# Performance work log

Hardware: AMD Instinct MI355X
Metric: run time of the kernel (lower is better)

## Reference

```python
import jax, jax.numpy as jnp
import numpy as np

EMBED = 32; HEADS = 4; HD = 8; FFN = 64; OBS = 64; CTX = 128; BATCH = 16
INIT_SCALE = 1.0 / np.sqrt(2.0 * 5.0)  # 1/sqrt(2*(3 spatial + 2 temporal))


def rmsnorm(x, w, eps=1e-6):
    return x / jnp.sqrt(jnp.mean(x * x, axis=-1, keepdims=True) + eps) * w


def rope_cache(T):
    theta = 1.0 / (10000.0 ** (jnp.arange(0, HD, 2, dtype=jnp.float32) / HD))
    freqs = jnp.arange(T, dtype=jnp.float32)[:, None] * theta[None, :]  # [T, HD//2]
    return jnp.cos(freqs), jnp.sin(freqs)


def apply_rope(x, cos, sin):
    half = x.shape[-1] // 2
    x1, x2 = x[..., :half], x[..., half:]
    c, s = cos[None, None], sin[None, None]  # broadcast over [B, H, T, HD//2]
    return jnp.concatenate([x1 * c - x2 * s, x2 * c + x1 * s], axis=-1)


def attn_block(x, Wq, Wk, Wv, Wo, Wg, Wval, Wout, norm4, qkn, cos=None, sin=None):
    B, S, W = x.shape
    h = rmsnorm(x, norm4[0])

    def proj(Wm):
        return jnp.einsum('bsw,dw->bsd', h, Wm).reshape(B, S, HEADS, HD).transpose(0, 2, 1, 3)

    q = rmsnorm(proj(Wq), qkn[0])
    k = rmsnorm(proj(Wk), qkn[1])
    v = proj(Wv)
    if cos is not None:
        q = apply_rope(q, cos, sin)
        k = apply_rope(k, cos, sin)
    scores = jnp.einsum('bhqd,bhkd->bhqk', q, k) / np.float32(np.sqrt(HD))
    o = jnp.einsum('bhqk,bhkd->bhqd', jax.nn.softmax(scores, axis=-1), v)
    o = o.transpose(0, 2, 1, 3).reshape(B, S, W)
    x = x + rmsnorm(jnp.einsum('bsw,dw->bsd', o, Wo), norm4[1])
    h2 = rmsnorm(x, norm4[2])
    ffn = jax.nn.silu(jnp.einsum('bsw,fw->bsf', h2, Wg)) * jnp.einsum('bsw,fw->bsf', h2, Wval)
    x = x + rmsnorm(jnp.einsum('bsf,wf->bsw', ffn, Wout), norm4[3])
    return x


def setup_inputs():
    key = jax.random.key(0)
    ks = iter(jax.random.split(key, 40))
    sd = 1.0 / np.sqrt(EMBED)
    inp = {
        'obs_seq': jax.random.normal(next(ks), (BATCH, CTX, OBS), jnp.float32),
        'W_val': jax.random.normal(next(ks), (EMBED, 1), jnp.float32),
        'b_val': jnp.zeros((EMBED,), jnp.float32),
        'input_norm_w': jnp.ones((EMBED,), jnp.float32),
        'dim_embed': jax.random.normal(next(ks), (OBS, EMBED), jnp.float32),
        'cls_tokens': jax.random.normal(next(ks), (3, EMBED), jnp.float32) * sd,
        'final_norm_w': jnp.ones((EMBED,), jnp.float32),
    }
    for pre, n in (('s', 3), ('t', 2)):
        inp[pre + '_Wq'] = jax.random.normal(next(ks), (n, EMBED, EMBED), jnp.float32) * sd
        inp[pre + '_Wk'] = jax.random.normal(next(ks), (n, EMBED, EMBED), jnp.float32) * sd
        inp[pre + '_Wv'] = jax.random.normal(next(ks), (n, EMBED, EMBED), jnp.float32) * sd
        inp[pre + '_Wo'] = jax.random.normal(next(ks), (n, EMBED, EMBED), jnp.float32) * (0.1 * INIT_SCALE * sd)
        inp[pre + '_Wg'] = jax.random.normal(next(ks), (n, FFN, EMBED), jnp.float32) * sd
        inp[pre + '_Wval'] = jax.random.normal(next(ks), (n, FFN, EMBED), jnp.float32) * sd
        inp[pre + '_Wout'] = jax.random.normal(next(ks), (n, EMBED, FFN), jnp.float32) * (INIT_SCALE / np.sqrt(FFN))
        inp[pre + '_norm4'] = jnp.ones((n, 4, EMBED), jnp.float32)
        inp[pre + '_qkn'] = jnp.ones((n, 2, HD), jnp.float32)
    return inp


def reference(obs_seq, W_val, b_val, input_norm_w, dim_embed, cls_tokens, final_norm_w,
              s_Wq, s_Wk, s_Wv, s_Wo, s_Wg, s_Wval, s_Wout, s_norm4, s_qkn,
              t_Wq, t_Wk, t_Wv, t_Wo, t_Wg, t_Wval, t_Wout, t_norm4, t_qkn):
    B, T, D = obs_seq.shape
    slots = D + 3
    # value_proj: Linear(1, EMBED) applied to each scalar feature
    tok = obs_seq[..., None] * W_val[:, 0] + b_val            # [B, T, D, EMBED]
    tok = tok + dim_embed[None, None]                          # dim id embedding
    cls = jnp.broadcast_to(cls_tokens[None, None], (B, T, 3, EMBED))
    tokens = rmsnorm(jnp.concatenate([tok, cls], axis=2), input_norm_w)  # [B,T,slots,EMBED]
    cos, sin = rope_cache(T)

    def spatial(tk, i):
        x = tk.reshape(B * T, slots, EMBED)
        x = attn_block(x, s_Wq[i], s_Wk[i], s_Wv[i], s_Wo[i], s_Wg[i], s_Wval[i], s_Wout[i], s_norm4[i], s_qkn[i])
        return x.reshape(B, T, slots, EMBED)

    def temporal(tk, i):
        x = tk.transpose(0, 2, 1, 3).reshape(B * slots, T, EMBED)
        x = attn_block(x, t_Wq[i], t_Wk[i], t_Wv[i], t_Wo[i], t_Wg[i], t_Wval[i], t_Wout[i], t_norm4[i], t_qkn[i], cos, sin)
        return x.reshape(B, slots, T, EMBED).transpose(0, 2, 1, 3)

    tokens = spatial(tokens, 0)
    tokens = temporal(tokens, 0)
    tokens = spatial(tokens, 1)
    tokens = temporal(tokens, 1)
    tokens = spatial(tokens, 2)
    tokens = rmsnorm(tokens, final_norm_w)
    last = tokens[:, -1]  # [B, slots, EMBED]
    return last[:, D], last[:, D + 1], last[:, D + 2]
```

## Files before the change

### kernel.cpp

```cpp
#include <hip/hip_runtime.h>

#define B_ 16
#define T_ 128
#define OBS_ 64
#define SLOTS_ 67
#define E_ 32
#define H_ 4
#define HD_ 8
#define FFN_ 64

typedef _Float16 h2 __attribute__((ext_vector_type(2)));
typedef _Float16 h4 __attribute__((ext_vector_type(4)));
typedef _Float16 h8 __attribute__((ext_vector_type(8)));
typedef __fp16 mh4 __attribute__((ext_vector_type(4)));
typedef __fp16 mh8 __attribute__((ext_vector_type(8)));
typedef float fx4 __attribute__((ext_vector_type(4)));
union H4u { h4 v; h2 h[2]; };

#define WBLK 10240
#define X16_BYTES (B_ * T_ * SLOTS_ * E_ * 2)
#define W16_BYTES (5 * WBLK * 2)
#define ROPE_OFF (X16_BYTES + W16_BYTES)
#define EMBED_BLOCKS ((B_ * T_ * SLOTS_ + 7) / 8)

__device__ __forceinline__ float red32(float v) {
  v += __shfl_xor(v, 16); v += __shfl_xor(v, 8); v += __shfl_xor(v, 4);
  v += __shfl_xor(v, 2);  v += __shfl_xor(v, 1);
  return v;
}
template <int CTRL>
__device__ __forceinline__ float dpp_add(float v) {
  int s = __builtin_amdgcn_update_dpp(0, __builtin_bit_cast(int, v), CTRL,
                                      0xF, 0xF, true);
  return v + __builtin_bit_cast(float, s);
}
__device__ __forceinline__ float red8(float v) {
  v = dpp_add<0xB1>(v);
  v = dpp_add<0x4E>(v);
  v = dpp_add<0x141>(v);
  return v;
}
__device__ __forceinline__ float bfly16(float v) {
  v = dpp_add<0xB1>(v);
  v = dpp_add<0x4E>(v);
  v = dpp_add<0x141>(v);
  v = dpp_add<0x140>(v);
  return v;
}
__device__ __forceinline__ h2 pkrtz(float x, float y) {
  return __builtin_bit_cast(h2, __builtin_amdgcn_cvt_pkrtz(x, y));
}
__device__ __forceinline__ float rcp_(float x) { return __builtin_amdgcn_rcpf(x); }
__device__ __forceinline__ float rsq_(float x) { return __builtin_amdgcn_rsqf(x); }
__device__ __forceinline__ fx4 mfma16(h8 a, h8 b, fx4 c) {
  return __builtin_amdgcn_mfma_f32_16x16x32_f16(
      __builtin_bit_cast(mh8, a), __builtin_bit_cast(mh8, b), c, 0, 0, 0);
}
__device__ __forceinline__ fx4 mfma16k16(h4 a, h4 b, fx4 c) {
  return __builtin_amdgcn_mfma_f32_16x16x16f16(
      __builtin_bit_cast(mh4, a), __builtin_bit_cast(mh4, b), c, 0, 0, 0);
}

__device__ __forceinline__ int sw32(int row, int col) {
  return row * 32 + (col ^ (((row >> 1) & 3) << 3));
}
__device__ __forceinline__ int sw64(int row, int col) {
  return row * 64 + (col ^ ((row & 7) << 3));
}

struct WPtrs {
  const float *sWq, *sWk, *sWv, *sWo, *sWg, *sWvl, *sWout;
  const float *tWq, *tWk, *tWv, *tWo, *tWg, *tWvl, *tWout;
};

#define CVT_BLOCKS 100

__global__ __launch_bounds__(256) void setup_kernel(
    WPtrs p, _Float16* __restrict__ dst,
    const float* __restrict__ obs, const float* __restrict__ Wval,
    const float* __restrict__ bval, const float* __restrict__ innw,
    const float* __restrict__ dimemb, const float* __restrict__ cls,
    float2* __restrict__ rope, _Float16* __restrict__ X) {
  if (blockIdx.x < CVT_BLOCKS) {
    int i = blockIdx.x * 256 + threadIdx.x;
    const int total_pairs = 5 * WBLK / 2;
    if (i >= total_pairs) return;
    int blk = i / (WBLK / 2);
    int f = (i % (WBLK / 2)) * 2;
    bool sp = blk < 3;
    int bi = sp ? blk : blk - 3;
    const float* src;
    int o;
    if (f < 1024)      { src = (sp ? p.sWq : p.tWq) + bi * 1024;  o = f; }
    else if (f < 2048) { src = (sp ? p.sWk : p.tWk) + bi * 1024;  o = f - 1024; }
    else if (f < 3072) { src = (sp ? p.sWv : p.tWv) + bi * 1024;  o = f - 2048; }
    else if (f < 4096) { src = (sp ? p.sWo : p.tWo) + bi * 1024;  o = f - 3072; }
    else if (f < 6144) { src = (sp ? p.sWg : p.tWg) + bi * 2048;  o = f - 4096; }
    else if (f < 8192) { src = (sp ? p.sWvl : p.tWvl) + bi * 2048; o = f - 6144; }
    else               { src = (sp ? p.sWout : p.tWout) + bi * 2048; o = f - 8192; }
    ((h2*)dst)[i] = pkrtz(src[o], src[o + 1]);
  } else if (blockIdx.x < CVT_BLOCKS + EMBED_BLOCKS) {
    int tok = (blockIdx.x - CVT_BLOCKS) * 8 + (threadIdx.x >> 5);
    int e = threadIdx.x & 31;
    const int total = B_ * T_ * SLOTS_;
    if (tok >= total) return;
    int slot = tok % SLOTS_;
    int bt = tok / SLOTS_;
    float v;
    if (slot < OBS_) {
      float o = obs[bt * OBS_ + slot];
      v = o * Wval[e] + bval[e] + dimemb[slot * E_ + e];
    } else {
      v = cls[(slot - OBS_) * E_ + e];
    }
    float ss = red32(v * v);
    X[tok * E_ + e] = (_Float16)(v * rsq_(ss * (1.0f / E_) + 1e-6f) * innw[e]);
  } else {
    for (int i = threadIdx.x; i < T_ * 4; i += 256) {
      int pos = i >> 2, j = i & 3;
      float th = __builtin_amdgcn_exp2f(-(float)j * 3.3219280948873623f);
      float sv, cv;
      __sincosf((float)pos * th, &sv, &cv);
      rope[i] = make_float2(cv, sv);
    }
  }
}

template <int SV, int SP, bool TEMPORAL, bool LAST>
__device__ __forceinline__ void block_body(
    _Float16* __restrict__ X, const _Float16* __restrict__ W16,
    const float* __restrict__ norm4, const float* __restrict__ qkn,
    const float2* __restrict__ rope, const float* __restrict__ fnw,
    float* __restrict__ out, int bid) {
  constexpr int MT = SP / 16;
  constexpr int MTW = (MT + 3) / 4;
  constexpr int VSTRIDE = TEMPORAL ? 128 : 168;
  constexpr int VROWS = TEMPORAL ? 32 : 33;
  __shared__ __align__(16) _Float16 smem[SP * 96 + VROWS * VSTRIDE];
  _Float16* hb = smem;
  _Float16* qb = smem + SP * 32;
  _Float16* kb = smem + SP * 64;
  _Float16* vT = smem + SP * 96;
  _Float16* ffnb = qb;

  const int tid = threadIdx.x;
  const int l = tid & 63, wv = tid >> 6;
  const int lm = l & 15, lq = l >> 4, hd = l & 7;

  auto vt_idx = [](int d, int s) {
    if (TEMPORAL) return d * 128 + (((s & ~15) ^ ((d & 7) << 4)) | (s & 15));
    return d * VSTRIDE + s;
  };

  int base, stride;
  if (TEMPORAL) {
    int b = bid / SLOTS_;
    int slot = bid % SLOTS_;
    base = (b * T_ * SLOTS_ + slot) * E_;
    stride = SLOTS_ * E_;
  } else {
    base = bid * 2 * SLOTS_ * E_;
    stride = E_;
  }

  const float nw0a = norm4[lm],      nw0b = norm4[16 + lm];
  const float nw1a = norm4[32 + lm], nw1b = norm4[48 + lm];
  const float nw2a = norm4[64 + lm], nw2b = norm4[80 + lm];
  const float nw3a = norm4[96 + lm], nw3b = norm4[112 + lm];
  const fx4 fz = {0.f, 0.f, 0.f, 0.f};
  const float qw = qkn[hd], kw = qkn[8 + hd];
  const float qscale = 0.35355339059327373f * 1.4426950408889634f;

  float xr[MTW][4][2];
#pragma unroll
  for (int t = 0; t < MTW; t++) {
    int mt = wv + 4 * t;
    if (mt < MT) {
#pragma unroll
      for (int r = 0; r < 4; r++) {
        int s = mt * 16 + lq * 4 + r;
        bool ok = (SV == SP) || (s < SV);
        int off = base + s * stride;
        xr[t][r][0] = ok ? (float)X[off + lm] : 0.f;
        xr[t][r][1] = ok ? (float)X[off + 16 + lm] : 0.f;
      }
    }
  }
#pragma unroll
  for (int t = 0; t < MTW; t++) {
    int mt = wv + 4 * t;
    if (mt < MT) {
#pragma unroll
      for (int r = 0; r < 4; r++) {
        int s = mt * 16 + lq * 4 + r;
        float p = bfly16(xr[t][r][0] * xr[t][r][0] + xr[t][r][1] * xr[t][r][1]);
        float inv = rsq_(p * (1.0f / E_) + 1e-6f);
        if (SV == SP || s < SV) {
          hb[sw32(s, lm)] = (_Float16)(xr[t][r][0] * inv * nw0a);
          hb[sw32(s, 16 + lm)] = (_Float16)(xr[t][r][1] * inv * nw0b);
        }
      }
    }
  }
  __syncthreads();

  for (int u = wv; u < MT * 2; u += 4) {
    const int mt = u >> 1, nt = u & 1;
    h8 aH = *(const h8*)(hb + sw32(mt * 16 + lm, lq * 8));
    float rc[4], rs[4];
    if (TEMPORAL) {
#pragma unroll
      for (int r = 0; r < 4; r++) {
        float2 cs = rope[(mt * 16 + lq * 4 + r) * 4 + (hd & 3)];
        rc[r] = cs.x; rs[r] = cs.y;
      }
    }
    const int d = nt * 16 + lm;
    h8 bq = *(const h8*)(W16 + (nt * 16 + lm) * 32 + lq * 8);
    h8 bk = *(const h8*)(W16 + 1024 + (nt * 16 + lm) * 32 + lq * 8);
    h8 bv = *(const h8*)(W16 + 2048 + (nt * 16 + lm) * 32 + lq * 8);
    fx4 aq = mfma16(aH, bq, fz);
    fx4 ak = mfma16(aH, bk, fz);
    fx4 av = mfma16(aH, bv, fz);
#pragma unroll
    for (int r = 0; r < 4; r++) {
      int s = mt * 16 + lq * 4 + r;
      float q1 = aq[r], k1 = ak[r];
      float qv = q1 * rsq_(red8(q1 * q1) * 0.125f + 1e-6f) * qw;
      float kv = k1 * rsq_(red8(k1 * k1) * 0.125f + 1e-6f) * kw;
      if (TEMPORAL) {
        float qp = __shfl_xor(qv, 4);
        float kp = __shfl_xor(kv, 4);
        qv = (hd < 4) ? (qv * rc[r] - qp * rs[r]) : (qv * rc[r] + qp * rs[r]);
        kv = (hd < 4) ? (kv * rc[r] - kp * rs[r]) : (kv * rc[r] + kp * rs[r]);
      }
      if (SV == SP || s < SV) {
        qb[sw32(s, d)] = (_Float16)(qv * qscale);
        kb[sw32(s, d)] = (_Float16)kv;
      }
    }
    const int s0 = mt * 16 + lq * 4;
    const int va = vt_idx(d, s0);
    if (SV == SP || s0 + 1 < SV) *(h2*)(vT + va) = pkrtz(av[0], av[1]);
    if (SV == SP || s0 + 3 < SV) *(h2*)(vT + va + 2) = pkrtz(av[2], av[3]);
  }
  if (!TEMPORAL) {
    for (int idx = tid; idx < 32 * 13; idx += 256) {
      int d = idx / 13, c = 2 * SLOTS_ + 2 * (idx % 13);
      *(h2*)(vT + d * VSTRIDE + c) = pkrtz(0.f, 0.f);
    }
    for (int idx = tid; idx < VSTRIDE / 2; idx += 256) {
      *(h2*)(vT + 32 * VSTRIDE + 2 * idx) = pkrtz(1.f, 1.f);
    }
  }
  __syncthreads();

  {
    const int h = wv;
    const h8 z8 = {};
    const h4 ones4 = {(_Float16)1.f, (_Float16)1.f, (_Float16)1.f, (_Float16)1.f};
    const bool vlane = (lm < 8);
    const int dv = h * 8 + (lm & 7);
    const int vrow = (!TEMPORAL && !vlane) ? 32 : dv;

    auto loadK = [&](int kt) {
      return *(const h8*)(kb + sw32(kt * 16 + lm, lq * 8));
    };
    auto loadV = [&](int kt) {
      h4 v = *(const h4*)(vT + vt_idx(vrow, kt * 16 + lq * 4));
      return (TEMPORAL && !vlane) ? ones4 : v;
    };
    auto loadQ = [&](int mt) {
      h8 b = *(const h8*)(qb + sw32(mt * 16 + lm, lq * 8));
      return (lq == h) ? b : z8;
    };
    auto maskx = [&](float x, int kidx, int mode, int q) {
      if (mode == 1) return (kidx < SLOTS_) ? x : 0.f;
      if (mode == 2) return (kidx >= SLOTS_) ? x : 0.f;
      if (mode == 3) return (kidx < 2 * SLOTS_) ? x : 0.f;
      if (mode == 4) {
        bool ok = (kidx < 2 * SLOTS_) && ((kidx < SLOTS_) == (q < SLOTS_));
        return ok ? x : 0.f;
      }
      return x;
    };
    auto pvstep = [&](const h4& av, int kt, int mode, int q, const fx4& sc,
                      fx4& oacc) {
      float ev[4];
#pragma unroll
      for (int r = 0; r < 4; r++) {
        int kidx = kt * 16 + lq * 4 + r;
        ev[r] = maskx(__builtin_amdgcn_exp2f(sc[r]), kidx, mode, q);
      }
      H4u pT;
      pT.h[0] = pkrtz(ev[0], ev[1]); pT.h[1] = pkrtz(ev[2], ev[3]);
      oacc = mfma16k16(av, pT.v, oacc);
    };
    auto finish = [&](int mt, fx4& oa) {
      int q = mt * 16 + lm;
      float lsum = __shfl_xor(oa[0], 32);
      float inv = rcp_(lsum);
      if (lq < 2 && (SV == SP || q < SV)) {
        H4u ov;
        ov.h[0] = pkrtz(oa[0] * inv, oa[1] * inv);
        ov.h[1] = pkrtz(oa[2] * inv, oa[3] * inv);
        *(h4*)(hb + sw32(q, h * 8 + lq * 4)) = ov.v;
      }
    };

    if (TEMPORAL) {
      h8 aK[MT]; h4 aV[MT];
#pragma unroll
      for (int kt = 0; kt < MT; kt++) { aK[kt] = loadK(kt); aV[kt] = loadV(kt); }
#pragma unroll
      for (int mtp = 0; mtp < MT / 2; mtp++) {
        h8 bQ0 = loadQ(2 * mtp), bQ1 = loadQ(2 * mtp + 1);
        fx4 o0 = fz, o1 = fz;
#pragma unroll
        for (int kt = 0; kt < MT; kt++) {
          fx4 s0 = mfma16(aK[kt], bQ0, fz);
          fx4 s1 = mfma16(aK[kt], bQ1, fz);
          pvstep(aV[kt], kt, 0, 0, s0, o0);
          pvstep(aV[kt], kt, 0, 0, s1, o1);
        }
        finish(2 * mtp, o0);
        finish(2 * mtp + 1, o1);
      }
    } else {
      {
        h8 aKw[5]; h4 aVw[5];
#pragma unroll
        for (int kt = 0; kt < 5; kt++) { aKw[kt] = loadK(kt); aVw[kt] = loadV(kt); }
#pragma unroll
        for (int mtp = 0; mtp < 2; mtp++) {
          h8 bQ0 = loadQ(2 * mtp), bQ1 = loadQ(2 * mtp + 1);
          fx4 o0 = fz, o1 = fz;
#pragma unroll
          for (int kt = 0; kt < 5; kt++) {
            int mode = (kt == 4) ? 1 : 0;
            fx4 s0 = mfma16(aKw[kt], bQ0, fz);
            fx4 s1 = mfma16(aKw[kt], bQ1, fz);
            pvstep(aVw[kt], kt, mode, 0, s0, o0);
            pvstep(aVw[kt], kt, mode, 0, s1, o1);
          }
          finish(2 * mtp, o0);
          finish(2 * mtp + 1, o1);
        }
      }
      {
        h8 aKw[9]; h4 aVw[9];
#pragma unroll
        for (int kt = 0; kt < 9; kt++) { aKw[kt] = loadK(kt); aVw[kt] = loadV(kt); }
        h8 bQ = loadQ(4);
        fx4 oa = fz;
        const int q = 4 * 16 + lm;
#pragma unroll
        for (int kt = 0; kt < 9; kt++) {
          fx4 sc = mfma16(aKw[kt], bQ, fz);
          pvstep(aVw[kt], kt, 4, q, sc, oa);
        }
        finish(4, oa);
      }
      {
        h8 aKw[5]; h4 aVw[5];
#pragma unroll
        for (int kt = 0; kt < 5; kt++) {
          aKw[kt] = loadK(kt + 4); aVw[kt] = loadV(kt + 4);
        }
#pragma unroll
        for (int mtp = 0; mtp < 2; mtp++) {
          int m0 = 5 + 2 * mtp;
          h8 bQ0 = loadQ(m0), bQ1 = loadQ(m0 + 1);
          fx4 o0 = fz, o1 = fz;
#pragma unroll
          for (int kt = 0; kt < 5; kt++) {
            int mode = (kt == 0) ? 2 : (kt == 4 ? 3 : 0);
            fx4 s0 = mfma16(aKw[kt], bQ0, fz);
            fx4 s1 = mfma16(aKw[kt], bQ1, fz);
            pvstep(aVw[kt], kt + 4, mode, 0, s0, o0);
            pvstep(aVw[kt], kt + 4, mode, 0, s1, o1);
          }
          finish(m0, o0);
          finish(m0 + 1, o1);
        }
      }
    }
  }
  __syncthreads();

#pragma unroll
  for (int t = 0; t < MTW; t++) {
    int mt = wv + 4 * t;
    if (mt < MT) {
      h8 aO = *(const h8*)(hb + sw32(mt * 16 + lm, lq * 8));
      h8 b0 = *(const h8*)(W16 + 3072 + lm * 32 + lq * 8);
      h8 b1 = *(const h8*)(W16 + 3072 + (16 + lm) * 32 + lq * 8);
      fx4 a0 = mfma16(aO, b0, fz);
      fx4 a1 = mfma16(aO, b1, fz);
#pragma unroll
      for (int r = 0; r < 4; r++) {
        int s = mt * 16 + lq * 4 + r;
        float p = bfly16(a0[r] * a0[r] + a1[r] * a1[r]);
        float inv = rsq_(p * (1.0f / E_) + 1e-6f);
        xr[t][r][0] += a0[r] * inv * nw1a;
        xr[t][r][1] += a1[r] * inv * nw1b;
        float q2 = bfly16(xr[t][r][0] * xr[t][r][0] + xr[t][r][1] * xr[t][r][1]);
        float inv2 = rsq_(q2 * (1.0f / E_) + 1e-6f);
        if (SV == SP || s < SV) {
          hb[sw32(s, lm)] = (_Float16)(xr[t][r][0] * inv2 * nw2a);
          hb[sw32(s, 16 + lm)] = (_Float16)(xr[t][r][1] * inv2 * nw2b);
        }
      }
    }
  }
  __syncthreads();

  for (int u = wv; u < MT * 4; u += 4) {
    const int mt = u >> 2, nt = u & 3;
    h8 aH2 = *(const h8*)(hb + sw32(mt * 16 + lm, lq * 8));
    h8 bg = *(const h8*)(W16 + 4096 + (nt * 16 + lm) * 32 + lq * 8);
    h8 bl = *(const h8*)(W16 + 6144 + (nt * 16 + lm) * 32 + lq * 8);
    fx4 g = mfma16(aH2, bg, fz);
    fx4 vvv = mfma16(aH2, bl, fz);
#pragma unroll
    for (int r = 0; r < 4; r++) {
      int s = mt * 16 + lq * 4 + r;
      if (SV == SP || s < SV) {
        float gg = g[r];
        float sg = gg * rcp_(1.0f + __builtin_amdgcn_exp2f(gg * -1.4426950408889634f));
        ffnb[sw64(s, nt * 16 + lm)] = (_Float16)(sg * vvv[r]);
      }
    }
  }
  __syncthreads();

#pragma unroll
  for (int t = 0; t < MTW; t++) {
    int mt = wv + 4 * t;
    if (mt < MT) {
      const int row = mt * 16 + lm;
      h8 a0 = *(const h8*)(ffnb + sw64(row, lq * 8));
      h8 a1 = *(const h8*)(ffnb + sw64(row, 32 + lq * 8));
      h8 b00 = *(const h8*)(W16 + 8192 + lm * 64 + lq * 8);
      h8 b01 = *(const h8*)(W16 + 8192 + lm * 64 + 32 + lq * 8);
      h8 b10 = *(const h8*)(W16 + 8192 + (16 + lm) * 64 + lq * 8);
      h8 b11 = *(const h8*)(W16 + 8192 + (16 + lm) * 64 + 32 + lq * 8);
      fx4 o0 = mfma16(a1, b01, mfma16(a0, b00, fz));
      fx4 o1 = mfma16(a1, b11, mfma16(a0, b10, fz));
#pragma unroll
      for (int r = 0; r < 4; r++) {
        int s = mt * 16 + lq * 4 + r;
        float p = bfly16(o0[r] * o0[r] + o1[r] * o1[r]);
        float inv = rsq_(p * (1.0f / E_) + 1e-6f);
        xr[t][r][0] += o0[r] * inv * nw3a;
        xr[t][r][1] += o1[r] * inv * nw3b;
        if (SV == SP || s < SV) {
          int off = base + s * stride;
          X[off + lm] = (_Float16)xr[t][r][0];
          X[off + 16 + lm] = (_Float16)xr[t][r][1];
        }
      }
      if (LAST && mt == MT - 1 && (bid & (T_ / 2 - 1)) == (T_ / 2 - 1)) {
        const int b = bid / (T_ / 2);
#pragma unroll
        for (int r = 0; r < 4; r++) {
          int s = mt * 16 + lq * 4 + r;
          int j = s - (SLOTS_ + OBS_);
          float p2 = bfly16(xr[t][r][0] * xr[t][r][0] + xr[t][r][1] * xr[t][r][1]);
          if (j >= 0 && j < 3) {
            float inv2 = rsq_(p2 * (1.0f / E_) + 1e-6f);
            out[j * (B_ * E_) + b * E_ + lm] = xr[t][r][0] * inv2 * fnw[lm];
            out[j * (B_ * E_) + b * E_ + 16 + lm] = xr[t][r][1] * inv2 * fnw[16 + lm];
          }
        }
      }
    }
  }
}

__global__ __launch_bounds__(256, 4) void attn_spatial_kernel(
    _Float16* __restrict__ X, const _Float16* __restrict__ W16,
    const float* __restrict__ norm4, const float* __restrict__ qkn) {
  block_body<2 * SLOTS_, 144, false, false>(X, W16, norm4, qkn, nullptr,
                                            nullptr, nullptr, blockIdx.x);
}

__global__ __launch_bounds__(256, 4) void attn_spatial_last_kernel(
    _Float16* __restrict__ X, const _Float16* __restrict__ W16,
    const float* __restrict__ norm4, const float* __restrict__ qkn,
    const float* __restrict__ fnw, float* __restrict__ out) {
  block_body<2 * SLOTS_, 144, false, true>(X, W16, norm4, qkn, nullptr,
                                           fnw, out, blockIdx.x);
}

__global__ __launch_bounds__(256, 4) void attn_temporal_kernel(
    _Float16* __restrict__ X, const _Float16* __restrict__ W16,
    const float* __restrict__ norm4, const float* __restrict__ qkn,
    const float2* __restrict__ rope) {
  block_body<T_, 128, true, false>(X, W16, norm4, qkn, rope,
                                   nullptr, nullptr, blockIdx.x);
}

extern "C" void kernel_launch(void* const* d_in, const int* in_sizes, int n_in,
                              void* d_out, int out_size, void* d_ws, size_t ws_size,
                              hipStream_t stream) {
  (void)in_sizes; (void)n_in; (void)out_size; (void)ws_size;
  const float* obs          = (const float*)d_in[0];
  const float* W_val        = (const float*)d_in[1];
  const float* b_val        = (const float*)d_in[2];
  const float* input_norm_w = (const float*)d_in[3];
  const float* dim_embed    = (const float*)d_in[4];
  const float* cls_tokens   = (const float*)d_in[5];
  const float* final_norm_w = (const float*)d_in[6];
  const float* s_n4   = (const float*)d_in[14];
  const float* s_qkn  = (const float*)d_in[15];
  const float* t_n4   = (const float*)d_in[23];
  const float* t_qkn  = (const float*)d_in[24];

  _Float16* X = (_Float16*)d_ws;
  _Float16* W16 = (_Float16*)((char*)d_ws + X16_BYTES);
  float2* rope = (float2*)((char*)d_ws + ROPE_OFF);
  float* out = (float*)d_out;

  WPtrs wp;
  wp.sWq   = (const float*)d_in[7];
  wp.sWk   = (const float*)d_in[8];
  wp.sWv   = (const float*)d_in[9];
  wp.sWo   = (const float*)d_in[10];
  wp.sWg   = (const float*)d_in[11];
  wp.sWvl  = (const float*)d_in[12];
  wp.sWout = (const float*)d_in[13];
  wp.tWq   = (const float*)d_in[16];
  wp.tWk   = (const float*)d_in[17];
  wp.tWv   = (const float*)d_in[18];
  wp.tWo   = (const float*)d_in[19];
  wp.tWg   = (const float*)d_in[20];
  wp.tWvl  = (const float*)d_in[21];
  wp.tWout = (const float*)d_in[22];

  setup_kernel<<<CVT_BLOCKS + EMBED_BLOCKS + 1, 256, 0, stream>>>(
      wp, W16, obs, W_val, b_val, input_norm_w, dim_embed, cls_tokens, rope, X);

  const int N4 = 4 * E_;
  const int QN = 2 * HD_;

#define SPATIAL(i)                                                     \
  attn_spatial_kernel<<<B_ * T_ / 2, 256, 0, stream>>>(                \
      X, W16 + (i)*WBLK, s_n4 + (i)*N4, s_qkn + (i)*QN)
#define TEMPORAL(i)                                                    \
  attn_temporal_kernel<<<B_ * SLOTS_, 256, 0, stream>>>(               \
      X, W16 + (3 + (i)) * WBLK, t_n4 + (i)*N4, t_qkn + (i)*QN, rope)

  SPATIAL(0);
  TEMPORAL(0);
  SPATIAL(1);
  TEMPORAL(1);
  attn_spatial_last_kernel<<<B_ * T_ / 2, 256, 0, stream>>>(
      X, W16 + 2 * WBLK, s_n4 + 2 * N4, s_qkn + 2 * QN, final_norm_w, out);

#undef SPATIAL
#undef TEMPORAL
}
```

Before: 281.8 us.

## Process one spatial group per block instead of packing two

The spatial kernel now gives each block a single 67-token group, padded to 80 rows, instead of packing two groups into 144 rows. Grid size doubles and per-block shared memory shrinks. The block-diagonal masking modes go away, and the middle tile's wasted cross-group work is no longer computed. The cost is lower MFMA tile utilisation (67 of 80 rows) and twice as many blocks to schedule.

Result: slower. 289.1 us (+2.6%).

```diff
diff --git a/kernel.cpp b/kernel.cpp
--- a/kernel.cpp
+++ b/kernel.cpp
@@ -134,7 +134,7 @@
     float* __restrict__ out, int bid) {
   constexpr int MT = SP / 16;
   constexpr int MTW = (MT + 3) / 4;
-  constexpr int VSTRIDE = TEMPORAL ? 128 : 168;
+  constexpr int VSTRIDE = TEMPORAL ? 128 : 88;
   constexpr int VROWS = TEMPORAL ? 32 : 33;
   __shared__ __align__(16) _Float16 smem[SP * 96 + VROWS * VSTRIDE];
   _Float16* hb = smem;
@@ -159,7 +159,7 @@
     base = (b * T_ * SLOTS_ + slot) * E_;
     stride = SLOTS_ * E_;
   } else {
-    base = bid * 2 * SLOTS_ * E_;
+    base = bid * SLOTS_ * E_;
     stride = E_;
   }
 
@@ -243,14 +243,15 @@
     const int va = vt_idx(d, s0);
     if (SV == SP || s0 + 1 < SV) *(h2*)(vT + va) = pkrtz(av[0], av[1]);
     if (SV == SP || s0 + 3 < SV) *(h2*)(vT + va + 2) = pkrtz(av[2], av[3]);
+    else if (s0 + 2 < SV)        *(h2*)(vT + va + 2) = pkrtz(av[2], 0.f);
   }
   if (!TEMPORAL) {
-    for (int idx = tid; idx < 32 * 13; idx += 256) {
-      int d = idx / 13, c = 2 * SLOTS_ + 2 * (idx % 13);
-      *(h2*)(vT + d * VSTRIDE + c) = pkrtz(0.f, 0.f);
-    }
-    for (int idx = tid; idx < VSTRIDE / 2; idx += 256) {
-      *(h2*)(vT + 32 * VSTRIDE + 2 * idx) = pkrtz(1.f, 1.f);
+    for (int idx = tid; idx < 32 * (SP - SV); idx += 256) {
+      int d = idx / (SP - SV), c = SV + idx % (SP - SV);
+      vT[d * VSTRIDE + c] = (_Float16)0.f;
+    }
+    for (int idx = tid; idx < SP; idx += 256) {
+      vT[32 * VSTRIDE + idx] = (_Float16)1.f;
     }
   }
   __syncthreads();
@@ -274,23 +275,17 @@
       h8 b = *(const h8*)(qb + sw32(mt * 16 + lm, lq * 8));
       return (lq == h) ? b : z8;
     };
-    auto maskx = [&](float x, int kidx, int mode, int q) {
+    auto maskx = [&](float x, int kidx, int mode) {
       if (mode == 1) return (kidx < SLOTS_) ? x : 0.f;
-      if (mode == 2) return (kidx >= SLOTS_) ? x : 0.f;
-      if (mode == 3) return (kidx < 2 * SLOTS_) ? x : 0.f;
-      if (mode == 4) {
-        bool ok = (kidx < 2 * SLOTS_) && ((kidx < SLOTS_) == (q < SLOTS_));
-        return ok ? x : 0.f;
-      }
       return x;
     };
-    auto pvstep = [&](const h4& av, int kt, int mode, int q, const fx4& sc,
+    auto pvstep = [&](const h4& av, int kt, int mode, const fx4& sc,
                       fx4& oacc) {
       float ev[4];
 #pragma unroll
       for (int r = 0; r < 4; r++) {
         int kidx = kt * 16 + lq * 4 + r;
-        ev[r] = maskx(__builtin_amdgcn_exp2f(sc[r]), kidx, mode, q);
+        ev[r] = maskx(__builtin_amdgcn_exp2f(sc[r]), kidx, mode);
       }
       H4u pT;
       pT.h[0] = pkrtz(ev[0], ev[1]); pT.h[1] = pkrtz(ev[2], ev[3]);
@@ -320,69 +315,42 @@
         for (int kt = 0; kt < MT; kt++) {
           fx4 s0 = mfma16(aK[kt], bQ0, fz);
           fx4 s1 = mfma16(aK[kt], bQ1, fz);
-          pvstep(aV[kt], kt, 0, 0, s0, o0);
-          pvstep(aV[kt], kt, 0, 0, s1, o1);
+          pvstep(aV[kt], kt, 0, s0, o0);
+          pvstep(aV[kt], kt, 0, s1, o1);
         }
         finish(2 * mtp, o0);
         finish(2 * mtp + 1, o1);
       }
     } else {
+      h8 aKw[5]; h4 aVw[5];
+#pragma unroll
+      for (int kt = 0; kt < 5; kt++) { aKw[kt] = loadK(kt); aVw[kt] = loadV(kt); }
+#pragma unroll
+      for (int mtp = 0; mtp < 2; mtp++) {
+        h8 bQ0 = loadQ(2 * mtp), bQ1 = loadQ(2 * mtp + 1);
+        fx4 o0 = fz, o1 = fz;
+#pragma unroll
+        for (int kt = 0; kt < 5; kt++) {
+          int mode = (kt == 4) ? 1 : 0;
+          fx4 s0 = mfma16(aKw[kt], bQ0, fz);
+          fx4 s1 = mfma16(aKw[kt], bQ1, fz);
+          pvstep(aVw[kt], kt, mode, s0, o0);
+          pvstep(aVw[kt], kt, mode, s1, o1);
+        }
+        finish(2 * mtp, o0);
+        finish(2 * mtp + 1, o1);
+      }
       {
-        h8 aKw[5]; h4 aVw[5];
-#pragma unroll
-        for (int kt = 0; kt < 5; kt++) { aKw[kt] = loadK(kt); aVw[kt] = loadV(kt); }
-#pragma unroll
-        for (int mtp = 0; mtp < 2; mtp++) {
-          h8 bQ0 = loadQ(2 * mtp), bQ1 = loadQ(2 * mtp + 1);
-          fx4 o0 = fz, o1 = fz;
-#pragma unroll
-          for (int kt = 0; kt < 5; kt++) {
-            int mode = (kt == 4) ? 1 : 0;
-            fx4 s0 = mfma16(aKw[kt], bQ0, fz);
-            fx4 s1 = mfma16(aKw[kt], bQ1, fz);
-            pvstep(aVw[kt], kt, mode, 0, s0, o0);
-            pvstep(aVw[kt], kt, mode, 0, s1, o1);
-          }
-          finish(2 * mtp, o0);
-          finish(2 * mtp + 1, o1);
-        }
-      }
-      {
-        h8 aKw[9]; h4 aVw[9];
-#pragma unroll
-        for (int kt = 0; kt < 9; kt++) { aKw[kt] = loadK(kt); aVw[kt] = loadV(kt); }
         h8 bQ = loadQ(4);
-        fx4 oa = fz;
-        const int q = 4 * 16 + lm;
-#pragma unroll
-        for (int kt = 0; kt < 9; kt++) {
+        fx4 oa = fz, ob = fz;
+#pragma unroll
+        for (int kt = 0; kt < 5; kt++) {
+          int mode = (kt == 4) ? 1 : 0;
           fx4 sc = mfma16(aKw[kt], bQ, fz);
-          pvstep(aVw[kt], kt, 4, q, sc, oa);
-        }
+          pvstep(aVw[kt], kt, mode, sc, (kt & 1) ? ob : oa);
+        }
+        oa = oa + ob;
         finish(4, oa);
-      }
-      {
-        h8 aKw[5]; h4 aVw[5];
-#pragma unroll
-        for (int kt = 0; kt < 5; kt++) {
-          aKw[kt] = loadK(kt + 4); aVw[kt] = loadV(kt + 4);
-        }
-#pragma unroll
-        for (int mtp = 0; mtp < 2; mtp++) {
-          int m0 = 5 + 2 * mtp;
-          h8 bQ0 = loadQ(m0), bQ1 = loadQ(m0 + 1);
-          fx4 o0 = fz, o1 = fz;
-#pragma unroll
-          for (int kt = 0; kt < 5; kt++) {
-            int mode = (kt == 0) ? 2 : (kt == 4 ? 3 : 0);
-            fx4 s0 = mfma16(aKw[kt], bQ0, fz);
-            fx4 s1 = mfma16(aKw[kt], bQ1, fz);
-            pvstep(aVw[kt], kt + 4, mode, 0, s0, o0);
-            pvstep(aVw[kt], kt + 4, mode, 0, s1, o1);
-          }
-          finish(m0, o0);
-          finish(m0 + 1, o1);
-        }
       }
     }
   }
@@ -460,12 +428,12 @@
           X[off + 16 + lm] = (_Float16)xr[t][r][1];
         }
       }
-      if (LAST && mt == MT - 1 && (bid & (T_ / 2 - 1)) == (T_ / 2 - 1)) {
-        const int b = bid / (T_ / 2);
+      if (LAST && mt == MT - 1 && (bid & (T_ - 1)) == (T_ - 1)) {
+        const int b = bid / T_;
 #pragma unroll
         for (int r = 0; r < 4; r++) {
           int s = mt * 16 + lq * 4 + r;
-          int j = s - (SLOTS_ + OBS_);
+          int j = s - OBS_;
           float p2 = bfly16(xr[t][r][0] * xr[t][r][0] + xr[t][r][1] * xr[t][r][1]);
           if (j >= 0 && j < 3) {
             float inv2 = rsq_(p2 * (1.0f / E_) + 1e-6f);
@@ -481,16 +449,16 @@
 __global__ __launch_bounds__(256, 4) void attn_spatial_kernel(
     _Float16* __restrict__ X, const _Float16* __restrict__ W16,
     const float* __restrict__ norm4, const float* __restrict__ qkn) {
-  block_body<2 * SLOTS_, 144, false, false>(X, W16, norm4, qkn, nullptr,
-                                            nullptr, nullptr, blockIdx.x);
+  block_body<SLOTS_, 80, false, false>(X, W16, norm4, qkn, nullptr,
+                                       nullptr, nullptr, blockIdx.x);
 }
 
 __global__ __launch_bounds__(256, 4) void attn_spatial_last_kernel(
     _Float16* __restrict__ X, const _Float16* __restrict__ W16,
     const float* __restrict__ norm4, const float* __restrict__ qkn,
     const float* __restrict__ fnw, float* __restrict__ out) {
-  block_body<2 * SLOTS_, 144, false, true>(X, W16, norm4, qkn, nullptr,
-                                           fnw, out, blockIdx.x);
+  block_body<SLOTS_, 80, false, true>(X, W16, norm4, qkn, nullptr,
+                                      fnw, out, blockIdx.x);
 }
 
 __global__ __launch_bounds__(256, 4) void attn_temporal_kernel(
@@ -545,7 +513,7 @@
   const int QN = 2 * HD_;
 
 #define SPATIAL(i)                                                     \
-  attn_spatial_kernel<<<B_ * T_ / 2, 256, 0, stream>>>(                \
+  attn_spatial_kernel<<<B_ * T_, 256, 0, stream>>>(                    \
       X, W16 + (i)*WBLK, s_n4 + (i)*N4, s_qkn + (i)*QN)
 #define TEMPORAL(i)                                                    \
   attn_temporal_kernel<<<B_ * SLOTS_, 256, 0, stream>>>(               \
@@ -555,7 +523,7 @@
   TEMPORAL(0);
   SPATIAL(1);
   TEMPORAL(1);
-  attn_spatial_last_kernel<<<B_ * T_ / 2, 256, 0, stream>>>(
+  attn_spatial_last_kernel<<<B_ * T_, 256, 0, stream>>>(
       X, W16 + 2 * WBLK, s_n4 + 2 * N4, s_qkn + 2 * QN, final_norm_w, out);
 
 #undef SPATIAL
```
